# Kernel tuning notes

Hardware: AMD Instinct MI355X
Metric: run time of the kernel (lower is better)

The kernel has to match this reference:

```python
import jax, jax.numpy as jnp
import numpy as np

D_MODEL = 1024
N_HEADS = 16
HEAD_DIM = D_MODEL // N_HEADS
SCALE = float(np.sqrt(HEAD_DIM))


def setup_inputs() -> dict:
    key = jax.random.key(0)
    ks = jax.random.split(key, 12)
    B, S, D = 4, 2048, D_MODEL
    std = 1.0 / np.sqrt(D)
    inp = {
        "query": jax.random.normal(ks[0], (B, S, D), jnp.float32),
        "key": jax.random.normal(ks[1], (B, S, D), jnp.float32),
        "value": jax.random.normal(ks[2], (B, S, D), jnp.float32),
        "wq_w": jax.random.normal(ks[3], (D, D), jnp.float32) * std,
        "wq_b": jnp.zeros((D,), jnp.float32),
        "wk_w": jax.random.normal(ks[4], (D, D), jnp.float32) * std,
        "wk_b": jnp.zeros((D,), jnp.float32),
        "wv_w": jax.random.normal(ks[5], (D, D), jnp.float32) * std,
        "wv_b": jnp.zeros((D,), jnp.float32),
        "fc_w": jax.random.normal(ks[6], (D, D), jnp.float32) * std,
        "fc_b": jnp.zeros((D,), jnp.float32),
    }
    return inp


def reference(query, key, value, wq_w, wq_b, wk_w, wk_b, wv_w, wv_b, fc_w, fc_b):
    B, S, D = query.shape
    H, Hd = N_HEADS, HEAD_DIM
    # QKV projections (torch Linear: x @ W.T + b)
    Q = query @ wq_w.T + wq_b
    K = key @ wk_w.T + wk_b
    V = value @ wv_w.T + wv_b
    # [B, H, S, Hd]
    Q = Q.reshape(B, S, H, Hd).transpose(0, 2, 1, 3)
    K = K.reshape(B, S, H, Hd).transpose(0, 2, 1, 3)
    V = V.reshape(B, S, H, Hd).transpose(0, 2, 1, 3)
    energy = jnp.einsum("bhqd,bhkd->bhqk", Q, K) / SCALE
    attention = jax.nn.softmax(energy, axis=-1)  # dropout=0 (eval)
    weighted = jnp.einsum("bhqk,bhkd->bhqd", attention, V)
    weighted = weighted.transpose(0, 2, 1, 3).reshape(B, S, D)
    output = weighted @ fc_w.T + fc_b
    return (output, attention)
```

## Files before the change

### kernel.cpp

```cpp
#include <hip/hip_runtime.h>
#include <hip/hip_bf16.h>
#include <math.h>

typedef __attribute__((ext_vector_type(8))) short short8;
typedef __attribute__((ext_vector_type(4))) short short4v;
typedef __attribute__((ext_vector_type(4))) float float4v;

#define GLD_LDS(g, l) __builtin_amdgcn_global_load_lds( \
    (const __attribute__((address_space(1))) void*)(g), \
    (__attribute__((address_space(3))) void*)(l), 16, 0, 0)

__device__ __forceinline__ short f2bf(float x) {
  __hip_bfloat16 h = __float2bfloat16(x);
  return __builtin_bit_cast(short, h);
}

__global__ __launch_bounds__(256) void cast3(
    const float4v* __restrict__ in0, const float4v* __restrict__ in1,
    const float4v* __restrict__ in2,
    short4v* __restrict__ o0, short4v* __restrict__ o1, short4v* __restrict__ o2,
    int n4)
{
  const float4v* in = blockIdx.y == 0 ? in0 : blockIdx.y == 1 ? in1 : in2;
  short4v* out = blockIdx.y == 0 ? o0 : blockIdx.y == 1 ? o1 : o2;
  int i = blockIdx.x * 256 + threadIdx.x;
  if (i < n4) {
    float4v v = in[i];
    short4v o;
    o[0] = f2bf(v[0]); o[1] = f2bf(v[1]); o[2] = f2bf(v[2]); o[3] = f2bf(v[3]);
    out[i] = o;
  }
}

__global__ __launch_bounds__(256) void cast4(
    const float4v* __restrict__ in0, const float4v* __restrict__ in1,
    const float4v* __restrict__ in2, const float4v* __restrict__ in3,
    short4v* __restrict__ o0, short4v* __restrict__ o1,
    short4v* __restrict__ o2, short4v* __restrict__ o3,
    int n4)
{
  const float4v* in = blockIdx.y == 0 ? in0 : blockIdx.y == 1 ? in1
                    : blockIdx.y == 2 ? in2 : in3;
  short4v* out = blockIdx.y == 0 ? o0 : blockIdx.y == 1 ? o1
               : blockIdx.y == 2 ? o2 : o3;
  int i = blockIdx.x * 256 + threadIdx.x;
  if (i < n4) {
    float4v v = in[i];
    short4v o;
    o[0] = f2bf(v[0]); o[1] = f2bf(v[1]); o[2] = f2bf(v[2]); o[3] = f2bf(v[3]);
    out[i] = o;
  }
}

template<int MODE>
__global__ __launch_bounds__(256) void gemm_bt(
    const short* __restrict__ A, const short* __restrict__ B,
    const float* __restrict__ bias, void* __restrict__ Cv,
    int M, int N, int K)
{
  __shared__ short As[2][128 * 64];
  __shared__ short Bs[2][128 * 64];
  const int tid = threadIdx.x;
  const int w = tid >> 6, lane = tid & 63;
  const int g = lane >> 4, cc = lane & 15;
  const int m0 = blockIdx.x * 128, n0 = blockIdx.y * 128;
  const int wr = (w >> 1) * 64, wc = (w & 1) * 64;

  float4v acc[4][4];
#pragma unroll
  for (int mi = 0; mi < 4; ++mi)
#pragma unroll
    for (int ni = 0; ni < 4; ++ni)
      acc[mi][ni] = (float4v){0.f, 0.f, 0.f, 0.f};

  const int cbase0 = w * 64;
  const int row_l[4] = {(cbase0 + lane) >> 3, (256 + cbase0 + lane) >> 3,
                        (512 + cbase0 + lane) >> 3, (768 + cbase0 + lane) >> 3};
  const int col_l = (lane & 7) * 8;

  auto stage = [&](int buf, int k0) {
#pragma unroll
    for (int i = 0; i < 4; ++i) {
      int cbase = i * 256 + cbase0;
      GLD_LDS(A + (long)(m0 + row_l[i]) * K + k0 + col_l, &As[buf][cbase * 8]);
      GLD_LDS(B + (long)(n0 + row_l[i]) * K + k0 + col_l, &Bs[buf][cbase * 8]);
    }
  };
  auto compute = [&](int buf) {
#pragma unroll
    for (int ks = 0; ks < 2; ++ks) {
      short8 af[4], bfr[4];
#pragma unroll
      for (int mi = 0; mi < 4; ++mi)
        af[mi] = *(const short8*)&As[buf][(wr + mi * 16 + cc) * 64 + ks * 32 + g * 8];
#pragma unroll
      for (int ni = 0; ni < 4; ++ni)
        bfr[ni] = *(const short8*)&Bs[buf][(wc + ni * 16 + cc) * 64 + ks * 32 + g * 8];
#pragma unroll
      for (int mi = 0; mi < 4; ++mi)
#pragma unroll
        for (int ni = 0; ni < 4; ++ni)
          acc[mi][ni] = __builtin_amdgcn_mfma_f32_16x16x32_bf16(
              af[mi], bfr[ni], acc[mi][ni], 0, 0, 0);
    }
  };

  stage(0, 0);
  __syncthreads();
#pragma unroll 1
  for (int k0 = 0; k0 < K; k0 += 128) {
    stage(1, k0 + 64);
    compute(0);
    __syncthreads();
    if (k0 + 128 < K) stage(0, k0 + 128);
    compute(1);
    __syncthreads();
  }

#pragma unroll
  for (int mi = 0; mi < 4; ++mi) {
#pragma unroll
    for (int ni = 0; ni < 4; ++ni) {
      int mb = m0 + wr + mi * 16 + g * 4;
      int nn = n0 + wc + ni * 16 + cc;
      float4v v = acc[mi][ni];
      if constexpr (MODE == 0) {
        float bb = bias[nn];
        __hip_bfloat16* C = (__hip_bfloat16*)Cv;
#pragma unroll
        for (int r = 0; r < 4; ++r)
          C[(long)(mb + r) * N + nn] = __float2bfloat16(v[r] + bb);
      } else if constexpr (MODE == 1) {
        __hip_bfloat16* C = (__hip_bfloat16*)Cv;
        long base = (long)(nn >> 11) * 2097152 + (nn & 2047);
#pragma unroll
        for (int r = 0; r < 4; ++r)
          C[(long)(mb + r) * 2048 + base] = __float2bfloat16(v[r] + bias[mb + r]);
      } else {
        float bb = bias[nn];
        float* C = (float*)Cv;
#pragma unroll
        for (int r = 0; r < 4; ++r)
          C[(long)(mb + r) * N + nn] = v[r] + bb;
      }
    }
  }
}

__global__ __launch_bounds__(256) void attn_fwd(
    const short* __restrict__ Qb, const short* __restrict__ Kb,
    const short* __restrict__ VTb, float* __restrict__ attn_out,
    __hip_bfloat16* __restrict__ Wout)
{
  __shared__ short plds[4][32][72];
  __shared__ float pldsF[4][32][65];
  const int S = 2048, D = 1024;
  const int bh = blockIdx.y, b = bh >> 4, h = bh & 15;
  const int tid = threadIdx.x, w = tid >> 6, lane = tid & 63;
  const int g = lane >> 4, cc = lane & 15;
  const int q0 = blockIdx.x * 128 + w * 32;

  const short* Qp = Qb + (long)b * S * D + h * 64;
  const short* Kp = Kb + (long)b * S * D + h * 64;
  const short* Vt = VTb + (long)bh * 64 * S;

  short8 qf[2][2];
#pragma unroll
  for (int mi = 0; mi < 2; ++mi)
#pragma unroll
    for (int ks = 0; ks < 2; ++ks)
      qf[mi][ks] = *(const short8*)(Qp + (long)(q0 + mi * 16 + cc) * D + ks * 32 + g * 8);

  float l[2] = {0.f, 0.f};
  const float C2 = 0.18033688011112042f;

#pragma unroll 1
  for (int kt = 0; kt < S; kt += 64) {
    float4v e[2][4];
#pragma unroll
    for (int mi = 0; mi < 2; ++mi)
#pragma unroll
      for (int ni = 0; ni < 4; ++ni) e[mi][ni] = (float4v){0.f, 0.f, 0.f, 0.f};
#pragma unroll
    for (int ks = 0; ks < 2; ++ks) {
      short8 kf[4];
#pragma unroll
      for (int ni = 0; ni < 4; ++ni)
        kf[ni] = *(const short8*)(Kp + (long)(kt + ni * 16 + cc) * D + ks * 32 + g * 8);
#pragma unroll
      for (int mi = 0; mi < 2; ++mi)
#pragma unroll
        for (int ni = 0; ni < 4; ++ni)
          e[mi][ni] = __builtin_amdgcn_mfma_f32_16x16x32_bf16(
              kf[ni], qf[mi][ks], e[mi][ni], 0, 0, 0);
    }
#pragma unroll
    for (int mi = 0; mi < 2; ++mi)
#pragma unroll
      for (int ni = 0; ni < 4; ++ni)
#pragma unroll
        for (int r = 0; r < 4; ++r)
          l[mi] += __builtin_exp2f(e[mi][ni][r] * C2);
  }
  float lrl[2];
#pragma unroll
  for (int mi = 0; mi < 2; ++mi) {
    float s = l[mi];
    s += __shfl_xor(s, 16);
    s += __shfl_xor(s, 32);
    lrl[mi] = -__log2f(s);
  }

  float4v Wacc[2][4];
#pragma unroll
  for (int mi = 0; mi < 2; ++mi)
#pragma unroll
    for (int ni = 0; ni < 4; ++ni) Wacc[mi][ni] = (float4v){0.f, 0.f, 0.f, 0.f};

  float* Arow = attn_out + (long)bh * S * S;
#pragma unroll 1
  for (int kt = 0; kt < S; kt += 64) {
    float4v e[2][4];
#pragma unroll
    for (int mi = 0; mi < 2; ++mi)
#pragma unroll
      for (int ni = 0; ni < 4; ++ni) e[mi][ni] = (float4v){0.f, 0.f, 0.f, 0.f};
#pragma unroll
    for (int ks = 0; ks < 2; ++ks) {
      short8 kf[4];
#pragma unroll
      for (int ni = 0; ni < 4; ++ni)
        kf[ni] = *(const short8*)(Kp + (long)(kt + ni * 16 + cc) * D + ks * 32 + g * 8);
#pragma unroll
      for (int mi = 0; mi < 2; ++mi)
#pragma unroll
        for (int ni = 0; ni < 4; ++ni)
          e[mi][ni] = __builtin_amdgcn_mfma_f32_16x16x32_bf16(
              kf[ni], qf[mi][ks], e[mi][ni], 0, 0, 0);
    }
#pragma unroll
    for (int mi = 0; mi < 2; ++mi) {
#pragma unroll
      for (int ni = 0; ni < 4; ++ni) {
        float4v pv;
#pragma unroll
        for (int r = 0; r < 4; ++r)
          pv[r] = __builtin_exp2f(__builtin_fmaf(e[mi][ni][r], C2, lrl[mi]));
        *(float4v*)&pldsF[w][mi * 16 + cc][ni * 16 + g * 4] = pv;
        short4v pb;
#pragma unroll
        for (int r = 0; r < 4; ++r) pb[r] = f2bf(pv[r]);
        *(short4v*)&plds[w][mi * 16 + cc][ni * 16 + g * 4] = pb;
      }
    }
#pragma unroll
    for (int j = 0; j < 8; ++j) {
      float4v pv4 = *(const float4v*)&pldsF[w][j * 4 + g][cc * 4];
      __builtin_nontemporal_store(
          pv4, (float4v*)(Arow + (long)(q0 + j * 4 + g) * S + kt + cc * 4));
    }
#pragma unroll
    for (int ks = 0; ks < 2; ++ks) {
      short8 pa[2], vf[4];
#pragma unroll
      for (int mi = 0; mi < 2; ++mi)
        pa[mi] = *(const short8*)&plds[w][mi * 16 + cc][ks * 32 + g * 8];
#pragma unroll
      for (int ni = 0; ni < 4; ++ni)
        vf[ni] = *(const short8*)(Vt + (long)(ni * 16 + cc) * S + kt + ks * 32 + g * 8);
#pragma unroll
      for (int mi = 0; mi < 2; ++mi)
#pragma unroll
        for (int ni = 0; ni < 4; ++ni)
          Wacc[mi][ni] = __builtin_amdgcn_mfma_f32_16x16x32_bf16(
              pa[mi], vf[ni], Wacc[mi][ni], 0, 0, 0);
    }
  }

#pragma unroll
  for (int mi = 0; mi < 2; ++mi)
#pragma unroll
    for (int ni = 0; ni < 4; ++ni)
#pragma unroll
      for (int r = 0; r < 4; ++r)
        Wout[(long)(b * S + q0 + mi * 16 + g * 4 + r) * D + h * 64 + ni * 16 + cc] =
            __float2bfloat16(Wacc[mi][ni][r]);
}

extern "C" void kernel_launch(void* const* d_in, const int* in_sizes, int n_in,
                              void* d_out, int out_size, void* d_ws, size_t ws_size,
                              hipStream_t stream) {
  const float* query = (const float*)d_in[0];
  const float* key   = (const float*)d_in[1];
  const float* value = (const float*)d_in[2];
  const float* wq_w  = (const float*)d_in[3];
  const float* wq_b  = (const float*)d_in[4];
  const float* wk_w  = (const float*)d_in[5];
  const float* wk_b  = (const float*)d_in[6];
  const float* wv_w  = (const float*)d_in[7];
  const float* wv_b  = (const float*)d_in[8];
  const float* fc_w  = (const float*)d_in[9];
  const float* fc_b  = (const float*)d_in[10];

  char* ws = (char*)d_ws;
  short* Qb  = (short*)(ws);
  short* Kb  = (short*)(ws + 16777216);
  short* VT  = (short*)(ws + 33554432);
  short* Wq  = (short*)(ws + 50331648);
  short* Wk  = (short*)(ws + 52428800);
  short* Wv  = (short*)(ws + 54525952);
  short* Wfc = (short*)(ws + 56623104);
  short* Xq  = (short*)(ws + 58720256);
  short* Xk  = (short*)(ws + 75497472);
  short* Xv  = (short*)(ws + 92274688);
  short* Wgt = Xq;

  float* out0 = (float*)d_out;
  float* attn_out = out0 + 8388608;

  cast3<<<dim3(8192, 3), 256, 0, stream>>>(
      (const float4v*)query, (const float4v*)key, (const float4v*)value,
      (short4v*)Xq, (short4v*)Xk, (short4v*)Xv, 2097152);
  cast4<<<dim3(1024, 4), 256, 0, stream>>>(
      (const float4v*)wq_w, (const float4v*)wk_w, (const float4v*)wv_w,
      (const float4v*)fc_w,
      (short4v*)Wq, (short4v*)Wk, (short4v*)Wv, (short4v*)Wfc, 262144);

  gemm_bt<0><<<dim3(64, 8), 256, 0, stream>>>(Xq, Wq, wq_b, Qb, 8192, 1024, 1024);
  gemm_bt<0><<<dim3(64, 8), 256, 0, stream>>>(Xk, Wk, wk_b, Kb, 8192, 1024, 1024);
  gemm_bt<1><<<dim3(8, 64), 256, 0, stream>>>(Wv, Xv, wv_b, VT, 1024, 8192, 1024);

  attn_fwd<<<dim3(16, 64), 256, 0, stream>>>(Qb, Kb, VT, attn_out,
                                             (__hip_bfloat16*)Wgt);

  gemm_bt<2><<<dim3(64, 8), 256, 0, stream>>>(Wgt, Wfc, fc_b, out0, 8192, 1024, 1024);
}
```

Baseline: 539.9 us.

## Enlarge GEMM tiles to 256x128 with 512 threads and prefetch K/V fragments in attention

```diff
diff --git a/kernel.cpp b/kernel.cpp
--- a/kernel.cpp
+++ b/kernel.cpp
@@ -53,18 +53,19 @@
 }
 
 template<int MODE>
-__global__ __launch_bounds__(256) void gemm_bt(
+__global__ __launch_bounds__(512) void gemm_bt(
     const short* __restrict__ A, const short* __restrict__ B,
     const float* __restrict__ bias, void* __restrict__ Cv,
     int M, int N, int K)
 {
-  __shared__ short As[2][128 * 64];
+  __shared__ short As[2][256 * 64];
   __shared__ short Bs[2][128 * 64];
   const int tid = threadIdx.x;
   const int w = tid >> 6, lane = tid & 63;
   const int g = lane >> 4, cc = lane & 15;
-  const int m0 = blockIdx.x * 128, n0 = blockIdx.y * 128;
-  const int wr = (w >> 1) * 64, wc = (w & 1) * 64;
+  const int m0 = blockIdx.x * 256, n0 = blockIdx.y * 128;
+  const int wr = (w >> 1) * 64;
+  const int wc = (w & 1) * 64;
 
   float4v acc[4][4];
 #pragma unroll
@@ -73,17 +74,21 @@
     for (int ni = 0; ni < 4; ++ni)
       acc[mi][ni] = (float4v){0.f, 0.f, 0.f, 0.f};
 
-  const int cbase0 = w * 64;
-  const int row_l[4] = {(cbase0 + lane) >> 3, (256 + cbase0 + lane) >> 3,
-                        (512 + cbase0 + lane) >> 3, (768 + cbase0 + lane) >> 3};
+  const int cb0 = w * 64;
   const int col_l = (lane & 7) * 8;
 
   auto stage = [&](int buf, int k0) {
 #pragma unroll
     for (int i = 0; i < 4; ++i) {
-      int cbase = i * 256 + cbase0;
-      GLD_LDS(A + (long)(m0 + row_l[i]) * K + k0 + col_l, &As[buf][cbase * 8]);
-      GLD_LDS(B + (long)(n0 + row_l[i]) * K + k0 + col_l, &Bs[buf][cbase * 8]);
+      int cbase = i * 512 + cb0;
+      int row = (cbase + lane) >> 3;
+      GLD_LDS(A + (long)(m0 + row) * K + k0 + col_l, &As[buf][cbase * 8]);
+    }
+#pragma unroll
+    for (int i = 0; i < 2; ++i) {
+      int cbase = i * 512 + cb0;
+      int row = (cbase + lane) >> 3;
+      GLD_LDS(B + (long)(n0 + row) * K + k0 + col_l, &Bs[buf][cbase * 8]);
     }
   };
   auto compute = [&](int buf) {
@@ -174,26 +179,36 @@
   float l[2] = {0.f, 0.f};
   const float C2 = 0.18033688011112042f;
 
+  short8 kc[2][4];
+#pragma unroll
+  for (int ks = 0; ks < 2; ++ks)
+#pragma unroll
+    for (int ni = 0; ni < 4; ++ni)
+      kc[ks][ni] = *(const short8*)(Kp + (long)(ni * 16 + cc) * D + ks * 32 + g * 8);
+
 #pragma unroll 1
   for (int kt = 0; kt < S; kt += 64) {
+    const int ktn = (kt + 64) & (S - 1);
+    short8 kn[2][4];
+#pragma unroll
+    for (int ks = 0; ks < 2; ++ks)
+#pragma unroll
+      for (int ni = 0; ni < 4; ++ni)
+        kn[ks][ni] = *(const short8*)(Kp + (long)(ktn + ni * 16 + cc) * D + ks * 32 + g * 8);
+
     float4v e[2][4];
 #pragma unroll
     for (int mi = 0; mi < 2; ++mi)
 #pragma unroll
       for (int ni = 0; ni < 4; ++ni) e[mi][ni] = (float4v){0.f, 0.f, 0.f, 0.f};
 #pragma unroll
-    for (int ks = 0; ks < 2; ++ks) {
-      short8 kf[4];
-#pragma unroll
-      for (int ni = 0; ni < 4; ++ni)
-        kf[ni] = *(const short8*)(Kp + (long)(kt + ni * 16 + cc) * D + ks * 32 + g * 8);
+    for (int ks = 0; ks < 2; ++ks)
 #pragma unroll
       for (int mi = 0; mi < 2; ++mi)
 #pragma unroll
         for (int ni = 0; ni < 4; ++ni)
           e[mi][ni] = __builtin_amdgcn_mfma_f32_16x16x32_bf16(
-              kf[ni], qf[mi][ks], e[mi][ni], 0, 0, 0);
-    }
+              kc[ks][ni], qf[mi][ks], e[mi][ni], 0, 0, 0);
 #pragma unroll
     for (int mi = 0; mi < 2; ++mi)
 #pragma unroll
@@ -201,6 +216,11 @@
 #pragma unroll
         for (int r = 0; r < 4; ++r)
           l[mi] += __builtin_exp2f(e[mi][ni][r] * C2);
+#pragma unroll
+    for (int ks = 0; ks < 2; ++ks)
+#pragma unroll
+      for (int ni = 0; ni < 4; ++ni)
+        kc[ks][ni] = kn[ks][ni];
   }
   float lrl[2];
 #pragma unroll
@@ -220,24 +240,28 @@
   float* Arow = attn_out + (long)bh * S * S;
 #pragma unroll 1
   for (int kt = 0; kt < S; kt += 64) {
+    const int ktn = (kt + 64) & (S - 1);
+    short8 kn[2][4];
+#pragma unroll
+    for (int ks = 0; ks < 2; ++ks)
+#pragma unroll
+      for (int ni = 0; ni < 4; ++ni)
+        kn[ks][ni] = *(const short8*)(Kp + (long)(ktn + ni * 16 + cc) * D + ks * 32 + g * 8);
+
     float4v e[2][4];
 #pragma unroll
     for (int mi = 0; mi < 2; ++mi)
 #pragma unroll
       for (int ni = 0; ni < 4; ++ni) e[mi][ni] = (float4v){0.f, 0.f, 0.f, 0.f};
 #pragma unroll
-    for (int ks = 0; ks < 2; ++ks) {
-      short8 kf[4];
-#pragma unroll
-      for (int ni = 0; ni < 4; ++ni)
-        kf[ni] = *(const short8*)(Kp + (long)(kt + ni * 16 + cc) * D + ks * 32 + g * 8);
+    for (int ks = 0; ks < 2; ++ks)
 #pragma unroll
       for (int mi = 0; mi < 2; ++mi)
 #pragma unroll
         for (int ni = 0; ni < 4; ++ni)
           e[mi][ni] = __builtin_amdgcn_mfma_f32_16x16x32_bf16(
-              kf[ni], qf[mi][ks], e[mi][ni], 0, 0, 0);
-    }
+              kc[ks][ni], qf[mi][ks], e[mi][ni], 0, 0, 0);
+
 #pragma unroll
     for (int mi = 0; mi < 2; ++mi) {
 #pragma unroll
@@ -253,28 +277,39 @@
         *(short4v*)&plds[w][mi * 16 + cc][ni * 16 + g * 4] = pb;
       }
     }
+
+    short8 vf[2][4];
+#pragma unroll
+    for (int ks = 0; ks < 2; ++ks)
+#pragma unroll
+      for (int ni = 0; ni < 4; ++ni)
+        vf[ks][ni] = *(const short8*)(Vt + (long)(ni * 16 + cc) * S + kt + ks * 32 + g * 8);
+
 #pragma unroll
     for (int j = 0; j < 8; ++j) {
       float4v pv4 = *(const float4v*)&pldsF[w][j * 4 + g][cc * 4];
       __builtin_nontemporal_store(
           pv4, (float4v*)(Arow + (long)(q0 + j * 4 + g) * S + kt + cc * 4));
     }
+
 #pragma unroll
     for (int ks = 0; ks < 2; ++ks) {
-      short8 pa[2], vf[4];
+      short8 pa[2];
 #pragma unroll
       for (int mi = 0; mi < 2; ++mi)
         pa[mi] = *(const short8*)&plds[w][mi * 16 + cc][ks * 32 + g * 8];
 #pragma unroll
-      for (int ni = 0; ni < 4; ++ni)
-        vf[ni] = *(const short8*)(Vt + (long)(ni * 16 + cc) * S + kt + ks * 32 + g * 8);
-#pragma unroll
       for (int mi = 0; mi < 2; ++mi)
 #pragma unroll
         for (int ni = 0; ni < 4; ++ni)
           Wacc[mi][ni] = __builtin_amdgcn_mfma_f32_16x16x32_bf16(
-              pa[mi], vf[ni], Wacc[mi][ni], 0, 0, 0);
-    }
+              pa[mi], vf[ks][ni], Wacc[mi][ni], 0, 0, 0);
+    }
+#pragma unroll
+    for (int ks = 0; ks < 2; ++ks)
+#pragma unroll
+      for (int ni = 0; ni < 4; ++ni)
+        kc[ks][ni] = kn[ks][ni];
   }
 
 #pragma unroll
@@ -326,12 +361,12 @@
       (const float4v*)fc_w,
       (short4v*)Wq, (short4v*)Wk, (short4v*)Wv, (short4v*)Wfc, 262144);
 
-  gemm_bt<0><<<dim3(64, 8), 256, 0, stream>>>(Xq, Wq, wq_b, Qb, 8192, 1024, 1024);
-  gemm_bt<0><<<dim3(64, 8), 256, 0, stream>>>(Xk, Wk, wk_b, Kb, 8192, 1024, 1024);
-  gemm_bt<1><<<dim3(8, 64), 256, 0, stream>>>(Wv, Xv, wv_b, VT, 1024, 8192, 1024);
+  gemm_bt<0><<<dim3(32, 8), 512, 0, stream>>>(Xq, Wq, wq_b, Qb, 8192, 1024, 1024);
+  gemm_bt<0><<<dim3(32, 8), 512, 0, stream>>>(Xk, Wk, wk_b, Kb, 8192, 1024, 1024);
+  gemm_bt<1><<<dim3(4, 64), 512, 0, stream>>>(Wv, Xv, wv_b, VT, 1024, 8192, 1024);
 
   attn_fwd<<<dim3(16, 64), 256, 0, stream>>>(Qb, Kb, VT, attn_out,
                                              (__hip_bfloat16*)Wgt);
 
-  gemm_bt<2><<<dim3(64, 8), 256, 0, stream>>>(Wgt, Wfc, fc_b, out0, 8192, 1024, 1024);
-}
+  gemm_bt<2><<<dim3(32, 8), 512, 0, stream>>>(Wgt, Wfc, fc_b, out0, 8192, 1024, 1024);
+}
```

Measured after the change: 548.2 us. No clear change (+1.5%).
